# Kernel optimization log

Measured on AMD Instinct MI355X. Metric: run time of the kernel, lower is better.

## Reference

```python
import jax, jax.numpy as jnp
import numpy as np

K_NBR = 64  # max_num_neighbors in radius()
M1, M2, M3 = 2048, 512, 512  # fps sample counts: 4096*0.5, 2048*0.25, 512*1.0
R1, R2, R3 = 0.2, 0.4, 1.0


def _fps_idx(pos, m):
    # Furthest point sampling, deterministic start at index 0. pos: [N,3] -> idx [m]
    d2 = jnp.sum((pos - pos[0]) ** 2, axis=-1)  # [N]

    def step(min_d2, _):
        nxt = jnp.argmax(min_d2).astype(jnp.int32)
        min_d2 = jnp.minimum(min_d2, jnp.sum((pos - pos[nxt]) ** 2, axis=-1))
        return min_d2, nxt

    _, rest = jax.lax.scan(step, d2, None, length=m - 1)
    return jnp.concatenate([jnp.zeros((1,), jnp.int32), rest])


def _ball_query(pos_src, pos_q, r, k):
    # Nearest up-to-k neighbors within radius r. Returns idx [M,k], valid mask [M,k].
    d2 = (jnp.sum(pos_q ** 2, -1)[:, None] + jnp.sum(pos_src ** 2, -1)[None, :]
          - 2.0 * pos_q @ pos_src.T)  # [M,N]
    neg = jnp.where(d2 <= r * r, -d2, -jnp.inf)
    vals, idx = jax.lax.top_k(neg, k)
    return idx, vals > -jnp.inf


def _sa_layer(x, pos, m, r, w1, b1, w2, b2):
    # x: [B,N,C], pos: [B,N,3] -> (x_new [B,m,Cout], pos_new [B,m,3])
    idx = jax.vmap(lambda p: _fps_idx(p, m))(pos)                     # [B,m]
    pos_q = jnp.take_along_axis(pos, idx[..., None], axis=1)         # [B,m,3]
    nbr, mask = jax.vmap(lambda s, q: _ball_query(s, q, r, K_NBR))(pos, pos_q)
    gather = jax.vmap(lambda a, i: a[i])                              # [N,C],[m,k]->[m,k,C]
    x_j = gather(x, nbr)                                              # [B,m,k,C]
    pos_j = gather(pos, nbr)                                          # [B,m,k,3]
    # PointNetConv message: MLP(concat(x_j, pos_j - pos_i)), max-aggregate
    msg = jnp.concatenate([x_j, pos_j - pos_q[:, :, None, :]], axis=-1)
    h = jnp.maximum(msg @ w1 + b1, 0.0) @ w2 + b2                     # [B,m,k,Cout]
    h = jnp.where(mask[..., None], h, -jnp.inf)
    out = jnp.max(h, axis=2)
    out = jnp.where(jnp.any(mask, axis=2, keepdims=True), out, 0.0)   # empty -> 0
    return out, pos_q


def setup_inputs() -> dict:
    key = jax.random.key(0)
    ks = jax.random.split(key, 8)
    B, N, C3 = 8, 4096, 128
    pos = jax.random.uniform(ks[0], (B, N, 3), jnp.float32)
    batch = jnp.repeat(jnp.arange(B, dtype=jnp.int32)[:, None], N, axis=1)

    def lin(k, ci, co):
        kw, kb = jax.random.split(k)
        s = 1.0 / np.sqrt(ci)
        return (jax.random.uniform(kw, (ci, co), jnp.float32, -s, s),
                jax.random.uniform(kb, (co,), jnp.float32, -s, s))

    w11, b11 = lin(ks[1], 3 + 3, 32)
    w12, b12 = lin(ks[2], 32, 32)
    w21, b21 = lin(ks[3], 32 + 3, 64)
    w22, b22 = lin(ks[4], 64, 64)
    w31, b31 = lin(ks[5], 64 + 3, C3)
    w32, b32 = lin(ks[6], C3, C3)
    return dict(pos=pos, batch=batch,
                w11=w11, b11=b11, w12=w12, b12=b12,
                w21=w21, b21=b21, w22=w22, b22=b22,
                w31=w31, b31=b31, w32=w32, b32=b32)


def reference(pos, batch, w11, b11, w12, b12, w21, b21, w22, b22, w31, b31, w32, b32):
    # Layer 1 uses positions as features (x = pos in encoder forward)
    x1, p1 = _sa_layer(pos, pos, M1, R1, w11, b11, w12, b12)
    x2, p2 = _sa_layer(x1, p1, M2, R2, w21, b21, w22, b22)
    x3, p3 = _sa_layer(x2, p2, M3, R3, w31, b31, w32, b32)
    return x3, p3, batch[:, :M3]
```

## Files before the change

### kernel.cpp

```cpp
#include <hip/hip_runtime.h>
#include <hip/hip_bf16.h>
#include <float.h>

typedef unsigned long long u64;

static __device__ __forceinline__ float d2_rn(float ax, float ay, float az,
                                              float bx, float by, float bz) {
  float dx = __fsub_rn(ax, bx), dy = __fsub_rn(ay, by), dz = __fsub_rn(az, bz);
  return __fadd_rn(__fadd_rn(__fmul_rn(dx, dx), __fmul_rn(dy, dy)), __fmul_rn(dz, dz));
}

template<int CTRL>
static __device__ __forceinline__ float dpp_f32(float x) {
  return __int_as_float(__builtin_amdgcn_update_dpp(0, __float_as_int(x), CTRL, 0xF, 0xF, true));
}

template<int CTRL>
static __device__ __forceinline__ int dpp_min_i32(int x) {
  int b = __builtin_amdgcn_update_dpp(0x7fffffff, x, CTRL, 0xF, 0xF, false);
  return x < b ? x : b;
}

template<int CTRL>
static __device__ __forceinline__ u64 dpp_u64(u64 x) {
  unsigned lo = (unsigned)__builtin_amdgcn_update_dpp(0, (int)(unsigned)x, CTRL, 0xF, 0xF, true);
  unsigned hi = (unsigned)__builtin_amdgcn_update_dpp(0, (int)(unsigned)(x >> 32), CTRL, 0xF, 0xF, true);
  return ((u64)hi << 32) | lo;
}

static __device__ __forceinline__ void merge2(u64& a1, u64& a2, u64 b1, u64 b2) {
  bool agt = a1 > b1;
  u64 m1 = agt ? a1 : b1;
  u64 lo = agt ? b1 : a1;
  u64 cs = agt ? a2 : b2;
  a1 = m1;
  a2 = lo > cs ? lo : cs;
}

template<int CTRL>
static __device__ __forceinline__ void merge_dpp(u64& a1, u64& a2) {
  u64 b1 = dpp_u64<CTRL>(a1);
  u64 b2 = dpp_u64<CTRL>(a2);
  merge2(a1, a2, b1, b2);
}

static __device__ __forceinline__ void pool16_top2(u64& a1, u64& a2) {
  merge_dpp<0xB1>(a1, a2);
  merge_dpp<0x4E>(a1, a2);
  merge_dpp<0x141>(a1, a2);
  merge_dpp<0x140>(a1, a2);
}

static __device__ __forceinline__ u64 bcast64(u64 x) {
  unsigned lo = (unsigned)__builtin_amdgcn_readfirstlane((int)(unsigned)x);
  unsigned hi = (unsigned)__builtin_amdgcn_readfirstlane((int)(x >> 32));
  return ((u64)hi << 32) | lo;
}

template<int CTRL>
static __device__ __forceinline__ void top2_step(float& v1, float& v2) {
  float b1 = dpp_f32<CTRL>(v1);
  float b2 = dpp_f32<CTRL>(v2);
  float m1 = fmaxf(v1, b1);
  float lo = fminf(v1, b1);
  v2 = fmaxf(lo, fmaxf(v2, b2));
  v1 = m1;
}

static __device__ __forceinline__ void wave_top2_vals(float& v1, float& v2) {
  top2_step<0xB1>(v1, v2);
  top2_step<0x4E>(v1, v2);
  top2_step<0x141>(v1, v2);
  top2_step<0x140>(v1, v2);
  top2_step<0x142>(v1, v2);
  top2_step<0x143>(v1, v2);
}

static __device__ __forceinline__ int wave_min_idx(int c) {
  c = dpp_min_i32<0xB1>(c);  c = dpp_min_i32<0x4E>(c);
  c = dpp_min_i32<0x141>(c); c = dpp_min_i32<0x140>(c);
  c = dpp_min_i32<0x142>(c); c = dpp_min_i32<0x143>(c);
  return __builtin_amdgcn_readlane(c, 63);
}

static __device__ __forceinline__ float readlane_f(float x, int l) {
  return __int_as_float(__builtin_amdgcn_readlane(__float_as_int(x), l));
}

static __device__ __forceinline__ void wave_recover_idx(float lv1, int li1, float lv2, int li2,
                                                        float s1, float s2, int lane,
                                                        int& i1g, int& i2g) {
  u64 b1 = __ballot(lv1 == s1);
  int lw;
  if (__popcll(b1) == 1) {
    lw = __ffsll(b1) - 1;
    i1g = __builtin_amdgcn_readlane(li1, lw);
  } else {
    i1g = wave_min_idx(lv1 == s1 ? li1 : 0x7fffffff);
    lw = __ffsll(__ballot(lv1 == s1 && li1 == i1g)) - 1;
  }
  float wlv = (lane == lw) ? lv2 : lv1;
  int   wli = (lane == lw) ? li2 : li1;
  u64 b2 = __ballot(wlv == s2);
  if (__popcll(b2) == 1) {
    i2g = __builtin_amdgcn_readlane(wli, __ffsll(b2) - 1);
  } else {
    i2g = wave_min_idx(wlv == s2 ? wli : 0x7fffffff);
  }
}

#define FPS_UPD(PP)                                                                    \
  { _Pragma("unroll")                                                                  \
    for (int k = 0; k < NPT; ++k) {                                                    \
      float m = md[k];                                                                 \
      _Pragma("unroll")                                                                \
      for (int mm = 0; mm < (PP); ++mm)                                                \
        m = fminf(m, d2_rn(px[k], py[k], pz[k], cx[mm], cy[mm], cz[mm]));              \
      md[k] = m; int j = tid + k * T;                                                  \
      if (m > v2) { if (m > v1) { v2=v1; i2=i1; v1=m; i1=j; } else { v2=m; i2=j; } }   \
    } }

template<int N, int M, int NPT, int T>
static __device__ void fps_body(const float* __restrict__ P, float* __restrict__ O,
                                char* smem) {
  constexpr int W = T / 64;
  static_assert(N == T * NPT, "layout");
  float4* pq = (float4*)smem;
  uint4* slots = (uint4*)(pq + N);
  const int tid = threadIdx.x;
  const int lane = tid & 63, wv = tid >> 6;

  for (int j = tid; j < N; j += T)
    pq[j] = make_float4(P[3 * j], P[3 * j + 1], P[3 * j + 2], 0.f);
  __syncthreads();

  const float4 c0 = pq[0];
  if (tid == 0) { O[0] = c0.x; O[1] = c0.y; O[2] = c0.z; }

  float md[NPT], px[NPT], py[NPT], pz[NPT];
  float v1 = -1.f, v2 = -1.f; int i1 = 0, i2 = 0;
  #pragma unroll
  for (int k = 0; k < NPT; ++k) {
    int j = tid + k * T;
    float4 p = pq[j];
    px[k] = p.x; py[k] = p.y; pz[k] = p.z;
    float m = d2_rn(p.x, p.y, p.z, c0.x, c0.y, c0.z);
    md[k] = m;
    if (m > v2) { if (m > v1) { v2=v1; i2=i1; v1=m; i1=j; } else { v2=m; i2=j; } }
  }

  {
    float r1 = v1, r2 = v2;
    wave_top2_vals(r1, r2);
    float s1 = readlane_f(r1, 63), s2 = readlane_f(r2, 63);
    int i1g, i2g;
    wave_recover_idx(v1, i1, v2, i2, s1, s2, lane, i1g, i2g);
    if (lane == 0)
      slots[wv] = make_uint4(__float_as_uint(s1), (unsigned)i1g,
                             __float_as_uint(s2), (unsigned)i2g);
  }

  int t = 1, phase = 0;
  while (t < M) {
    __syncthreads();
    uint4 sp = slots[phase * W + (lane & (W - 1))];
    u64 key;
    {
      unsigned vb = (lane & 8) ? sp.z : sp.x;
      unsigned ib = (lane & 8) ? sp.w : sp.y;
      key = ((u64)vb << 32) | (unsigned)(~ib);
    }
    if (lane >= 16) key = 0;
    u64 a1 = key, a2 = 0;
    pool16_top2(a1, a2);
    a1 = bcast64(a1); a2 = bcast64(a2);
    const int j1 = (int)(~(unsigned)a1);
    const int j2 = (int)(~(unsigned)a2);
    const float v2f = __uint_as_float((unsigned)(a2 >> 32));
    u64 b1 = (key == a1 || key == a2) ? 0ull : key, b2 = 0;
    pool16_top2(b1, b2);
    b1 = bcast64(b1); b2 = bcast64(b2);

    const float4 c1 = pq[j1];
    const float4 c2 = pq[j2];

    const int room = M - t;
    float cx[4], cy[4], cz[4];
    cx[0] = c1.x; cy[0] = c1.y; cz[0] = c1.z;
    int p = 1;
    unsigned seen = 1u << ((j1 & (T - 1)) >> 6);
    bool capped = false;
    bool hit = (room >= 2) && (v2f > 0.f) &&
               (d2_rn(c2.x, c2.y, c2.z, c1.x, c1.y, c1.z) >= v2f);
    if (hit) {
      cx[1] = c2.x; cy[1] = c2.y; cz[1] = c2.z; p = 2;
      unsigned wb = 1u << ((j2 & (T - 1)) >> 6);
      if (seen & wb) capped = true;
      seen |= wb;
      if (!capped && room >= 3) {
        const float v3 = __uint_as_float((unsigned)(b1 >> 32));
        if (v3 > 0.f) {
          const int j3 = (int)(~(unsigned)b1);
          const float4 c3 = pq[j3];
          if (d2_rn(c3.x, c3.y, c3.z, c1.x, c1.y, c1.z) >= v3 &&
              d2_rn(c3.x, c3.y, c3.z, c2.x, c2.y, c2.z) >= v3) {
            cx[2] = c3.x; cy[2] = c3.y; cz[2] = c3.z; p = 3;
            unsigned wb3 = 1u << ((j3 & (T - 1)) >> 6);
            if (seen & wb3) capped = true;
            seen |= wb3;
            if (!capped && room >= 4) {
              const float v4 = __uint_as_float((unsigned)(b2 >> 32));
              if (v4 > 0.f) {
                const int j4 = (int)(~(unsigned)b2);
                const float4 c4 = pq[j4];
                if (d2_rn(c4.x, c4.y, c4.z, c1.x, c1.y, c1.z) >= v4 &&
                    d2_rn(c4.x, c4.y, c4.z, c2.x, c2.y, c2.z) >= v4 &&
                    d2_rn(c4.x, c4.y, c4.z, c3.x, c3.y, c3.z) >= v4) {
                  cx[3] = c4.x; cy[3] = c4.y; cz[3] = c4.z; p = 4;
                }
              }
            }
          }
        }
      }
    }

    if (tid == 0) {
      #pragma unroll
      for (int mm = 0; mm < 4; ++mm)
        if (mm < p) {
          O[3 * (t + mm)] = cx[mm]; O[3 * (t + mm) + 1] = cy[mm]; O[3 * (t + mm) + 2] = cz[mm];
        }
    }

    v1 = -1.f; v2 = -1.f; i1 = 0; i2 = 0;
    switch (p) {
      case 1:  FPS_UPD(1); break;
      case 2:  FPS_UPD(2); break;
      case 3:  FPS_UPD(3); break;
      default: FPS_UPD(4); break;
    }

    {
      float r1b = v1, r2b = v2;
      wave_top2_vals(r1b, r2b);
      float s1 = readlane_f(r1b, 63), s2 = readlane_f(r2b, 63);
      int i1g, i2g;
      wave_recover_idx(v1, i1, v2, i2, s1, s2, lane, i1g, i2g);
      if (lane == 0)
        slots[(phase ^ 1) * W + wv] = make_uint4(__float_as_uint(s1), (unsigned)i1g,
                                                 __float_as_uint(s2), (unsigned)i2g);
    }
    phase ^= 1;
    t += p;
  }
}

template<int N, int M, int NPT>
__global__ __launch_bounds__(512, 2) void fps_kernel(const float* __restrict__ pos,
                                                     float* __restrict__ out) {
  __shared__ __align__(16) char smem[16 * N + 2 * 8 * 16];
  fps_body<N, M, NPT, 512>(pos + (size_t)blockIdx.x * N * 3,
                           out + (size_t)blockIdx.x * M * 3, smem);
}

template<int C, int H>
__global__ void g_kernel(const float* __restrict__ x, const float* __restrict__ pos,
                         const float* __restrict__ W, float* __restrict__ g, int rows) {
  int idx = blockIdx.x * 256 + threadIdx.x;
  if (idx >= rows * H) return;
  int row = idx / H, h = idx - row * H;
  const float* xr = x + (size_t)row * C;
  const float* pr = pos + (size_t)row * 3;
  float acc = 0.f;
  for (int c = 0; c < C; ++c) acc = fmaf(xr[c], W[c * H + h], acc);
  #pragma unroll
  for (int c = 0; c < 3; ++c) acc = fmaf(pr[c], W[(C + c) * H + h], acc);
  g[idx] = acc;
}

template<int N, int H, int C, int T>
constexpr int sa_smem_bytes() {
  constexpr int TPS = C / 2, SG = T / TPS, JT = SG * 4, STRIDE = JT + 4;
  constexpr int SCR = (SG * C > 512) ? SG * C : 512;
  return H * C * 2 + N * 4 + H * 4 + STRIDE * H * 4 + SCR * 4 + 64 * 4 + 8 * 4 + 8 * 4;
}

template<int N, int H, int C, int QB, int T>
static __device__ void sa_body(const float* __restrict__ srcb,
                               const float* __restrict__ gb,
                               const float* __restrict__ qposb,
                               const float* __restrict__ W2, const float* __restrict__ b1v,
                               const float* __restrict__ W1p, const float* __restrict__ b2v,
                               float r2, int M, float* __restrict__ outb, int qtile,
                               char* smem) {
  constexpr int TPS = C / 2;
  constexpr int SG  = T / TPS;
  constexpr int JT  = SG * 4;
  constexpr int STRIDE = JT + 4;
  constexpr int SCR = (SG * C > 512) ? SG * C : 512;
  const int tid = threadIdx.x;
  const int sgi = tid / TPS;
  const int c2 = 2 * (tid - sgi * TPS);

  __hip_bfloat16* sW2h = (__hip_bfloat16*)smem;
  float* sD2  = (float*)(smem + H * C * 2);
  float* sT   = sD2 + N;
  float* sHj  = sT + H;
  float* sScr = sHj + STRIDE * H;
  int*   sNbr = (int*)(sScr + SCR);
  int*   sWS  = sNbr + 64;
  int*   sIv  = sWS + 8;
  float* sFv  = (float*)(sIv + 6);

  int*   sHist  = (int*)sScr;
  float* sCand  = sScr + 256;
  int*   sCandI = (int*)(sScr + 320);
  float* sRed   = sScr;

  for (int e = tid; e < H * C; e += T) sW2h[e] = __float2bfloat16(W2[e]);

  for (int qi = 0; qi < QB; ++qi) {
    const int i = qtile * QB + qi;
    const float* qp = qposb + (size_t)i * 3;
    const float qx = qp[0], qy = qp[1], qz = qp[2];
    const float qq = __fadd_rn(__fadd_rn(__fmul_rn(qx, qx), __fmul_rn(qy, qy)),
                               __fmul_rn(qz, qz));
    if (tid < H)
      sT[tid] = fmaf(qx, W1p[tid], fmaf(qy, W1p[H + tid], fmaf(qz, W1p[2 * H + tid], -b1v[tid])));
    if (tid == 0) { sIv[0] = 0; sIv[1] = 0; sIv[2] = 0; }
    if (tid < 256) sHist[tid] = 0;
    __syncthreads();

    int lc = 0;
    for (int j = tid; j < N; j += T) {
      float sx = srcb[3 * j], sy = srcb[3 * j + 1], sz = srcb[3 * j + 2];
      float ss  = __fadd_rn(__fadd_rn(__fmul_rn(sx, sx), __fmul_rn(sy, sy)), __fmul_rn(sz, sz));
      float dot = __fadd_rn(__fadd_rn(__fmul_rn(qx, sx), __fmul_rn(qy, sy)), __fmul_rn(qz, sz));
      float d2  = __fsub_rn(__fadd_rn(qq, ss), __fmul_rn(2.0f, dot));
      sD2[j] = d2;
      lc += (d2 <= r2) ? 1 : 0;
    }
    #pragma unroll
    for (int off = 32; off > 0; off >>= 1) lc += __shfl_xor(lc, off, 64);
    if ((tid & 63) == 0) atomicAdd(&sIv[0], lc);
    __syncthreads();
    const int cnt = sIv[0];

    float tauv; int taui;
    if (cnt <= 64) {
      tauv = r2; taui = 0x7fffffff;
    } else {
      const float scale = 256.0f / r2;
      for (int j = tid; j < N; j += T) {
        float d2 = sD2[j];
        if (d2 <= r2) {
          int bin = (int)(d2 * scale);
          bin = bin < 0 ? 0 : (bin > 255 ? 255 : bin);
          atomicAdd(&sHist[bin], 1);
        }
      }
      __syncthreads();
      int cbin = (tid < 256) ? sHist[tid] : 0;
      int lane = tid & 63, wvi = tid >> 6;
      int v = cbin;
      #pragma unroll
      for (int off = 1; off < 64; off <<= 1) {
        int o = __shfl_up(v, off, 64);
        if (lane >= off) v += o;
      }
      if (lane == 63) sWS[wvi] = v;
      __syncthreads();
      int wadd = 0;
      for (int w = 0; w < wvi; ++w) wadd += sWS[w];
      int incl = v + wadd, excl = incl - cbin;
      if (tid < 256 && excl < 64 && incl >= 64) { sIv[3] = tid; sIv[4] = excl; }
      __syncthreads();
      const int bstar = sIv[3];
      const int kneed = 64 - sIv[4];
      for (int j = tid; j < N; j += T) {
        float d2 = sD2[j];
        if (d2 <= r2) {
          int bin = (int)(d2 * scale);
          bin = bin < 0 ? 0 : (bin > 255 ? 255 : bin);
          if (bin == bstar) {
            int p = atomicAdd(&sIv[2], 1);
            if (p < 64) { sCand[p] = d2; sCandI[p] = j; }
          }
        }
      }
      __syncthreads();
      if (tid == 0) {
        int nc = sIv[2] < 64 ? sIv[2] : 64;
        for (int a = 1; a < nc; ++a) {
          float dv = sCand[a]; int di = sCandI[a];
          int p = a - 1;
          while (p >= 0 && (sCand[p] > dv || (sCand[p] == dv && sCandI[p] > di))) {
            sCand[p + 1] = sCand[p]; sCandI[p + 1] = sCandI[p]; --p;
          }
          sCand[p + 1] = dv; sCandI[p + 1] = di;
        }
        int kk = (kneed < nc ? kneed : nc) - 1; if (kk < 0) kk = 0;
        sFv[0] = sCand[kk]; sIv[5] = sCandI[kk];
      }
      __syncthreads();
      tauv = sFv[0]; taui = sIv[5];
    }

    for (int j = tid; j < N; j += T) {
      float d2 = sD2[j];
      if (d2 < tauv || (d2 == tauv && j <= taui)) {
        int p = atomicAdd(&sIv[1], 1);
        if (p < 64) sNbr[p] = j;
      }
    }
    __syncthreads();
    const int nn = sIv[1] < 64 ? sIv[1] : 64;

    float m0 = -FLT_MAX, m1 = -FLT_MAX;
    for (int t0 = 0; t0 < nn; t0 += JT) {
      int jt = nn - t0; if (jt > JT) jt = JT;
      __syncthreads();
      for (int e = tid; e < JT * H; e += T) {
        int jj = e / H, h = e - jj * H;
        float hv = 0.f;
        if (jj < jt) {
          int j = sNbr[t0 + jj];
          hv = gb[(size_t)j * H + h] - sT[h];
          hv = hv > 0.f ? hv : 0.f;
        }
        sHj[h * STRIDE + jj] = hv;
      }
      __syncthreads();
      float a0 = 0, a1 = 0, a2 = 0, a3 = 0, c0 = 0, c1 = 0, c2a = 0, c3 = 0;
      const int jbase = sgi * 4;
      for (int h = 0; h < H; ++h) {
        float4 hv = *reinterpret_cast<const float4*>(&sHj[h * STRIDE + jbase]);
        __hip_bfloat162 wp = *reinterpret_cast<const __hip_bfloat162*>(&sW2h[h * C + c2]);
        float wx = __bfloat162float(wp.x), wy = __bfloat162float(wp.y);
        a0 = fmaf(hv.x, wx, a0); a1 = fmaf(hv.y, wx, a1);
        a2 = fmaf(hv.z, wx, a2); a3 = fmaf(hv.w, wx, a3);
        c0 = fmaf(hv.x, wy, c0); c1 = fmaf(hv.y, wy, c1);
        c2a = fmaf(hv.z, wy, c2a); c3 = fmaf(hv.w, wy, c3);
      }
      if (jbase + 0 < jt) { m0 = fmaxf(m0, a0); m1 = fmaxf(m1, c0); }
      if (jbase + 1 < jt) { m0 = fmaxf(m0, a1); m1 = fmaxf(m1, c1); }
      if (jbase + 2 < jt) { m0 = fmaxf(m0, a2); m1 = fmaxf(m1, c2a); }
      if (jbase + 3 < jt) { m0 = fmaxf(m0, a3); m1 = fmaxf(m1, c3); }
    }
    __syncthreads();
    sRed[sgi * C + c2]     = m0;
    sRed[sgi * C + c2 + 1] = m1;
    __syncthreads();
    if (tid < TPS) {
      int c = 2 * tid;
      float M0 = sRed[c], M1 = sRed[c + 1];
      #pragma unroll
      for (int s2 = 1; s2 < SG; ++s2) {
        M0 = fmaxf(M0, sRed[s2 * C + c]);
        M1 = fmaxf(M1, sRed[s2 * C + c + 1]);
      }
      float o0 = nn > 0 ? M0 + b2v[c]     : 0.f;
      float o1 = nn > 0 ? M1 + b2v[c + 1] : 0.f;
      float* orow = outb + (size_t)i * C;
      orow[c] = o0; orow[c + 1] = o1;
    }
    __syncthreads();
  }
}

template<int N, int H, int C, int QB>
__global__ __launch_bounds__(256) void sa_kernel(
    const float* __restrict__ src, const float* __restrict__ g,
    const float* __restrict__ qpos, const float* __restrict__ W2,
    const float* __restrict__ b1v, const float* __restrict__ W1p,
    const float* __restrict__ b2v, float r2, int M, float* __restrict__ out) {
  __shared__ __align__(16) char smem[sa_smem_bytes<N, H, C, 256>()];
  const int b = blockIdx.y;
  sa_body<N, H, C, QB, 256>(src + (size_t)b * N * 3, g + (size_t)b * N * H,
                            qpos + (size_t)b * M * 3, W2, b1v, W1p, b2v, r2, M,
                            out + (size_t)b * M * C, blockIdx.x, smem);
}

template<int NF, int MF, int NPTF, int NS, int HS, int CS, int QB, int SAB>
__global__ __launch_bounds__(512, 2) void fused_kernel(
    const float* __restrict__ fsrc, float* __restrict__ fdst,
    const float* __restrict__ src, const float* __restrict__ g,
    const float* __restrict__ qpos, const float* __restrict__ W2,
    const float* __restrict__ b1v, const float* __restrict__ W1p,
    const float* __restrict__ b2v, float r2, int M, float* __restrict__ out) {
  constexpr int FPS_BYTES = 16 * NF + 2 * 8 * 16;
  constexpr int SA_BYTES  = sa_smem_bytes<NS, HS, CS, 512>();
  constexpr int SMEM = FPS_BYTES > SA_BYTES ? FPS_BYTES : SA_BYTES;
  __shared__ __align__(16) char smem[SMEM];
  if (blockIdx.x < 8) {
    __builtin_amdgcn_s_setprio(3);
    fps_body<NF, MF, NPTF, 512>(fsrc + (size_t)blockIdx.x * NF * 3,
                                fdst + (size_t)blockIdx.x * MF * 3, smem);
    return;
  }
  const int bi = blockIdx.x - 8;
  const int qt = bi % SAB;
  const int b  = bi / SAB;
  sa_body<NS, HS, CS, QB, 512>(src + (size_t)b * NS * 3, g + (size_t)b * NS * HS,
                               qpos + (size_t)b * M * 3, W2, b1v, W1p, b2v, r2, M,
                               out + (size_t)b * M * CS, qt, smem);
}

__global__ void tail_kernel(const float* __restrict__ p3, float* __restrict__ d_out) {
  int i = blockIdx.x * 256 + threadIdx.x;
  if (i < 8 * 512 * 3) d_out[524288 + i] = p3[i];
  if (i < 8 * 512)     d_out[536576 + i] = (float)(i >> 9);
}

extern "C" void kernel_launch(void* const* d_in, const int* in_sizes, int n_in,
                              void* d_out, int out_size, void* d_ws, size_t ws_size,
                              hipStream_t stream) {
  (void)in_sizes; (void)n_in; (void)out_size; (void)ws_size;
  const float* pos = (const float*)d_in[0];
  const float* w11 = (const float*)d_in[2];
  const float* b11 = (const float*)d_in[3];
  const float* w12 = (const float*)d_in[4];
  const float* b12 = (const float*)d_in[5];
  const float* w21 = (const float*)d_in[6];
  const float* b21 = (const float*)d_in[7];
  const float* w22 = (const float*)d_in[8];
  const float* b22 = (const float*)d_in[9];
  const float* w31 = (const float*)d_in[10];
  const float* b31 = (const float*)d_in[11];
  const float* w32 = (const float*)d_in[12];
  const float* b32 = (const float*)d_in[13];

  float* ws = (float*)d_ws;
  float* p1 = ws; ws += 8 * 2048 * 3;
  float* p2 = ws; ws += 8 * 512 * 3;
  float* p3 = ws; ws += 8 * 512 * 3;
  float* g1 = ws; ws += 8 * 4096 * 32;
  float* x1 = ws; ws += 8 * 2048 * 32;
  float* g2 = ws; ws += 8 * 2048 * 64;
  float* x2 = ws; ws += 8 * 512 * 64;
  float* g3 = ws; ws += 8 * 512 * 128;
  float* x3 = (float*)d_out;

  g_kernel<3, 32><<<dim3(8 * 4096 * 32 / 256), dim3(256), 0, stream>>>(pos, pos, w11, g1, 8 * 4096);
  fps_kernel<4096, 2048, 8><<<dim3(8), dim3(512), 0, stream>>>(pos, p1);

  fused_kernel<2048, 512, 4, 4096, 32, 32, 8, 256><<<dim3(8 + 8 * 256), dim3(512), 0, stream>>>(
      p1, p2, pos, g1, p1, w12, b11, w11 + 3 * 32, b12, 0.04f, 2048, x1);

  g_kernel<32, 64><<<dim3(8 * 2048 * 64 / 256), dim3(256), 0, stream>>>(x1, p1, w21, g2, 8 * 2048);

  fused_kernel<512, 512, 1, 2048, 64, 64, 8, 64><<<dim3(8 + 8 * 64), dim3(512), 0, stream>>>(
      p2, p3, p1, g2, p2, w22, b21, w21 + 32 * 64, b22, 0.16f, 512, x2);

  g_kernel<64, 128><<<dim3(8 * 512 * 128 / 256), dim3(256), 0, stream>>>(x2, p2, w31, g3, 8 * 512);

  sa_kernel<512, 128, 128, 8><<<dim3(64, 8), dim3(256), 0, stream>>>(
      p2, g3, p3, w32, b31, w31 + 64 * 128, b32, 1.0f, 512, x3);

  tail_kernel<<<dim3(48), dim3(256), 0, stream>>>(p3, (float*)d_out);
}
```

Baseline: 2.188 ms.

## Accept more FPS multi-pick candidates via rank test and template max picks

Broadens the speculative multi-point acceptance in furthest point sampling. A candidate whose distance to the already chosen points falls below its old value can still be accepted if its updated key would outrank the next pooled candidate. The change also adds a MAXP template parameter so the fused kernel's FPS path limits itself to two picks per iteration and skips the second top-2 pool reduction. More picks per iteration means fewer serial block-wide iterations, at the cost of extra comparisons, and the rank-based acceptance must exactly reproduce the sequential argmax order.

```diff
diff --git a/kernel.cpp b/kernel.cpp
--- a/kernel.cpp
+++ b/kernel.cpp
@@ -120,7 +120,7 @@
       if (m > v2) { if (m > v1) { v2=v1; i2=i1; v1=m; i1=j; } else { v2=m; i2=j; } }   \
     } }
 
-template<int N, int M, int NPT, int T>
+template<int N, int M, int NPT, int T, int MAXP>
 static __device__ void fps_body(const float* __restrict__ P, float* __restrict__ O,
                                 char* smem) {
   constexpr int W = T / 64;
@@ -177,9 +177,12 @@
     const int j1 = (int)(~(unsigned)a1);
     const int j2 = (int)(~(unsigned)a2);
     const float v2f = __uint_as_float((unsigned)(a2 >> 32));
-    u64 b1 = (key == a1 || key == a2) ? 0ull : key, b2 = 0;
-    pool16_top2(b1, b2);
-    b1 = bcast64(b1); b2 = bcast64(b2);
+    u64 b1 = 0, b2 = 0;
+    if constexpr (MAXP >= 3) {
+      b1 = (key == a1 || key == a2) ? 0ull : key;
+      pool16_top2(b1, b2);
+      b1 = bcast64(b1); b2 = bcast64(b2);
+    }
 
     const float4 c1 = pq[j1];
     const float4 c2 = pq[j2];
@@ -189,38 +192,56 @@
     cx[0] = c1.x; cy[0] = c1.y; cz[0] = c1.z;
     int p = 1;
     unsigned seen = 1u << ((j1 & (T - 1)) >> 6);
-    bool capped = false;
-    bool hit = (room >= 2) && (v2f > 0.f) &&
-               (d2_rn(c2.x, c2.y, c2.z, c1.x, c1.y, c1.z) >= v2f);
-    if (hit) {
-      cx[1] = c2.x; cy[1] = c2.y; cz[1] = c2.z; p = 2;
+    bool stop = false;
+
+    if (room >= 2 && v2f > 0.f) {
+      float dd = d2_rn(c2.x, c2.y, c2.z, c1.x, c1.y, c1.z);
+      bool acc = (dd >= v2f);
       unsigned wb = 1u << ((j2 & (T - 1)) >> 6);
-      if (seen & wb) capped = true;
-      seen |= wb;
-      if (!capped && room >= 3) {
+      if constexpr (MAXP >= 3) {
+        if (!acc && !(seen & wb)) {
+          u64 kr = ((u64)__float_as_uint(dd) << 32) | (unsigned)(~j2);
+          acc = (kr > b1);
+        }
+      }
+      if (acc) {
+        cx[1] = c2.x; cy[1] = c2.y; cz[1] = c2.z; p = 2;
+        if (seen & wb) stop = true;
+        seen |= wb;
+      } else stop = true;
+    } else stop = true;
+
+    if constexpr (MAXP >= 3) {
+      if (!stop && room >= 3) {
         const float v3 = __uint_as_float((unsigned)(b1 >> 32));
         if (v3 > 0.f) {
           const int j3 = (int)(~(unsigned)b1);
           const float4 c3 = pq[j3];
-          if (d2_rn(c3.x, c3.y, c3.z, c1.x, c1.y, c1.z) >= v3 &&
-              d2_rn(c3.x, c3.y, c3.z, c2.x, c2.y, c2.z) >= v3) {
+          float mn = fminf(d2_rn(c3.x, c3.y, c3.z, c1.x, c1.y, c1.z),
+                           d2_rn(c3.x, c3.y, c3.z, cx[1], cy[1], cz[1]));
+          bool acc = (mn >= v3);
+          unsigned wb3 = 1u << ((j3 & (T - 1)) >> 6);
+          if (!acc && !(seen & wb3)) {
+            float m3 = fminf(v3, mn);
+            u64 kr = ((u64)__float_as_uint(m3) << 32) | (unsigned)(~j3);
+            acc = (kr > b2);
+          }
+          if (acc) {
             cx[2] = c3.x; cy[2] = c3.y; cz[2] = c3.z; p = 3;
-            unsigned wb3 = 1u << ((j3 & (T - 1)) >> 6);
-            if (seen & wb3) capped = true;
+            if (seen & wb3) stop = true;
             seen |= wb3;
-            if (!capped && room >= 4) {
-              const float v4 = __uint_as_float((unsigned)(b2 >> 32));
-              if (v4 > 0.f) {
-                const int j4 = (int)(~(unsigned)b2);
-                const float4 c4 = pq[j4];
-                if (d2_rn(c4.x, c4.y, c4.z, c1.x, c1.y, c1.z) >= v4 &&
-                    d2_rn(c4.x, c4.y, c4.z, c2.x, c2.y, c2.z) >= v4 &&
-                    d2_rn(c4.x, c4.y, c4.z, c3.x, c3.y, c3.z) >= v4) {
-                  cx[3] = c4.x; cy[3] = c4.y; cz[3] = c4.z; p = 4;
-                }
-              }
-            }
-          }
+          } else stop = true;
+        } else stop = true;
+      }
+      if (!stop && room >= 4) {
+        const float v4 = __uint_as_float((unsigned)(b2 >> 32));
+        if (v4 > 0.f) {
+          const int j4 = (int)(~(unsigned)b2);
+          const float4 c4 = pq[j4];
+          float mn = fminf(fminf(d2_rn(c4.x, c4.y, c4.z, c1.x, c1.y, c1.z),
+                                 d2_rn(c4.x, c4.y, c4.z, cx[1], cy[1], cz[1])),
+                           d2_rn(c4.x, c4.y, c4.z, cx[2], cy[2], cz[2]));
+          if (mn >= v4) { cx[3] = c4.x; cy[3] = c4.y; cz[3] = c4.z; p = 4; }
         }
       }
     }
@@ -260,8 +281,8 @@
 __global__ __launch_bounds__(512, 2) void fps_kernel(const float* __restrict__ pos,
                                                      float* __restrict__ out) {
   __shared__ __align__(16) char smem[16 * N + 2 * 8 * 16];
-  fps_body<N, M, NPT, 512>(pos + (size_t)blockIdx.x * N * 3,
-                           out + (size_t)blockIdx.x * M * 3, smem);
+  fps_body<N, M, NPT, 512, 4>(pos + (size_t)blockIdx.x * N * 3,
+                              out + (size_t)blockIdx.x * M * 3, smem);
 }
 
 template<int C, int H>
@@ -495,8 +516,8 @@
   __shared__ __align__(16) char smem[SMEM];
   if (blockIdx.x < 8) {
     __builtin_amdgcn_s_setprio(3);
-    fps_body<NF, MF, NPTF, 512>(fsrc + (size_t)blockIdx.x * NF * 3,
-                                fdst + (size_t)blockIdx.x * MF * 3, smem);
+    fps_body<NF, MF, NPTF, 512, 2>(fsrc + (size_t)blockIdx.x * NF * 3,
+                                   fdst + (size_t)blockIdx.x * MF * 3, smem);
     return;
   }
   const int bi = blockIdx.x - 8;
```

Measured after the change: 2.126 ms. 2.8% less time.
